# Performance work log

Measured on AMD Instinct MI355X. Metric: run time of the kernel, lower is better.

The kernel has to match this reference:

```python
import jax, jax.numpy as jnp
import numpy as np

B, S, E, H = 4, 1024, 1024, 16
HD = E // H


def setup_inputs() -> dict:
    key = jax.random.key(0)
    ks = jax.random.split(key, 5)
    x = jax.random.normal(ks[0], (B, S, E), dtype=jnp.float32)
    # causal mask: True = masked (filled with -inf), as in masked_fill_
    mask = jnp.triu(jnp.ones((S, S), dtype=bool), k=1)
    in_proj_weight = jax.random.normal(ks[1], (3 * E, E), dtype=jnp.float32) * (E ** -0.5)
    in_proj_bias = jax.random.normal(ks[2], (3 * E,), dtype=jnp.float32) * 0.02
    out_w = jax.random.normal(ks[3], (E, E), dtype=jnp.float32) * (E ** -0.5)
    out_b = jax.random.normal(ks[4], (E,), dtype=jnp.float32) * 0.02
    return {"x": x, "mask": mask, "in_proj_weight": in_proj_weight,
            "in_proj_bias": in_proj_bias, "out_w": out_w, "out_b": out_b}


def reference(x, mask, in_proj_weight, in_proj_bias, out_w, out_b):
    scaling = HD ** -0.5
    # fused QKV projection (self-attention path: qkv_same)
    qkv = jnp.einsum('bse,fe->bsf', x, in_proj_weight) + in_proj_bias  # [B,S,3E]
    q, k, v = jnp.split(qkv, 3, axis=-1)
    # split heads -> [B,H,S,HD]
    def heads(t):
        return t.reshape(B, S, H, HD).transpose(0, 2, 1, 3)
    q, k, v = heads(q), heads(k), heads(v)
    scores = jnp.einsum('bhsd,bhtd->bhst', q, k) * scaling  # [B,H,S,S]
    scores = jnp.where(mask[None, None, :, :], -jnp.inf, scores)
    att = jax.nn.softmax(scores, axis=-1)  # dropout p=0.0 (eval)
    out = jnp.einsum('bhst,bhtd->bhsd', att, v)  # [B,H,S,HD]
    out = out.transpose(0, 2, 1, 3).reshape(B, S, E)  # concat heads
    out = jnp.einsum('bse,fe->bsf', out, out_w) + out_b
    att_weights = att.reshape(B * H, S, S)
    return out, att_weights
```

## Files before the change

kernel.cpp:

```cpp
#include <hip/hip_runtime.h>
#include <hip/hip_bf16.h>
#include <stdint.h>

#define NH 16
#define SEQ 1024
#define EMB 1024
#define HDIM 64
#define BATCH 4
#define SPAD 1032

typedef float f32x4 __attribute__((ext_vector_type(4)));
typedef short bf16x8 __attribute__((ext_vector_type(8)));
typedef short bf16x4 __attribute__((ext_vector_type(4)));

static __device__ __forceinline__ short f2bf(float f) {
  union { float f; uint32_t u; } v; v.f = f;
  uint32_t r = (v.u + 0x7FFF + ((v.u >> 16) & 1)) >> 16;
  return (short)(uint16_t)r;
}
static __device__ __forceinline__ float bf2f(short h) {
  union { uint32_t u; float f; } v; v.u = ((uint32_t)(uint16_t)h) << 16;
  return v.f;
}

static __device__ __forceinline__ void gload_lds16(const void* g, void* l) {
  __builtin_amdgcn_global_load_lds(
      (const __attribute__((address_space(1))) void*)g,
      (__attribute__((address_space(3))) void*)l, 16, 0, 0);
}

static __device__ __forceinline__ void cvt8(const float* s, short* d) {
  const float4* sv = (const float4*)s;
  float4 a = sv[0], b = sv[1];
  bf16x8 o;
  o[0] = f2bf(a.x); o[1] = f2bf(a.y); o[2] = f2bf(a.z); o[3] = f2bf(a.w);
  o[4] = f2bf(b.x); o[5] = f2bf(b.y); o[6] = f2bf(b.z); o[7] = f2bf(b.w);
  *(bf16x8*)d = o;
}

__global__ void cvt3_kernel(const float* __restrict__ x, const float* __restrict__ w,
                            const float* __restrict__ o, short* __restrict__ xb,
                            short* __restrict__ wb, short* __restrict__ ob) {
  int i = (blockIdx.x * blockDim.x + threadIdx.x) * 8;
  if (i < 4194304) {
    cvt8(x + i, xb + i);
  } else if (i < 7340032) {
    cvt8(w + (i - 4194304), wb + (i - 4194304));
  } else {
    cvt8(o + (i - 7340032), ob + (i - 7340032));
  }
}

__global__ __launch_bounds__(256) void transpose_v(const short* __restrict__ v,
                                                   short* __restrict__ vt) {
  __shared__ short t[64][72];
  const int tid = threadIdx.x;
  const int bh = blockIdx.y;
  const int sb = blockIdx.x * 64;
  const int row = tid >> 2;
  const int c0 = (tid & 3) * 16;
  const short* src = v + ((size_t)(bh * SEQ + sb + row)) * HDIM + c0;
  *(bf16x8*)&t[row][c0] = *(const bf16x8*)src;
  *(bf16x8*)&t[row][c0 + 8] = *(const bf16x8*)(src + 8);
  __syncthreads();
  bf16x8 o0, o1;
#pragma unroll
  for (int i = 0; i < 8; ++i) o0[i] = t[c0 + i][row];
#pragma unroll
  for (int i = 0; i < 8; ++i) o1[i] = t[c0 + 8 + i][row];
  short* dst = vt + ((size_t)(bh * HDIM + row)) * SEQ + sb + c0;
  *(bf16x8*)dst = o0;
  *(bf16x8*)(dst + 8) = o1;
}

#define STAGE_QKV(bb, kk0)                                                     \
  {                                                                            \
    _Pragma("unroll") for (int c = 0; c < 2; ++c) {                            \
      int oo = o + c * 1024;                                                   \
      int row = oo >> 6;                                                       \
      int scol = (oo & 63) ^ ((row & 3) << 4);                                 \
      gload_lds16((const char*)A + ((size_t)(row0 + row) * K + (kk0)) * 2 + scol, \
                  (char*)As[bb] + (w * 2 + c) * 1024);                         \
      gload_lds16((const char*)Bm + ((size_t)(col0 + row) * K + (kk0)) * 2 + scol,\
                  (char*)Bs[bb] + (w * 2 + c) * 1024);                         \
    }                                                                          \
  }

#define COMPUTE_QKV(bb)                                                        \
  {                                                                            \
    bf16x8 af[4], bfr[4];                                                      \
    const int kbo = (l4 * 16) ^ ((l15 & 3) << 4);                              \
    _Pragma("unroll") for (int i = 0; i < 4; ++i) {                            \
      af[i] = *(const bf16x8*)((const char*)As[bb] + (wr * 64 + i * 16 + l15) * 64 + kbo); \
      bfr[i] = *(const bf16x8*)((const char*)Bs[bb] + (wc * 64 + i * 16 + l15) * 64 + kbo); \
    }                                                                          \
    _Pragma("unroll") for (int i = 0; i < 4; ++i)                              \
      _Pragma("unroll") for (int j = 0; j < 4; ++j)                            \
        acc[i][j] = __builtin_amdgcn_mfma_f32_16x16x32_bf16(af[i], bfr[j], acc[i][j], 0, 0, 0); \
  }

__global__ __launch_bounds__(256) void gemm_qkv(
    const short* __restrict__ A, const short* __restrict__ Bm,
    const float* __restrict__ bias, short* __restrict__ qkvws) {
  __shared__ short As[2][128 * 32];
  __shared__ short Bs[2][128 * 32];
  const int tid = threadIdx.x;
  const int w = tid >> 6, l = tid & 63;
  const int l15 = l & 15, l4 = l >> 4;
  const int wr = w >> 1, wc = w & 1;
  const int row0 = blockIdx.x * 128;
  const int col0 = blockIdx.y * 128;
  const int K = EMB;

  f32x4 acc[4][4] = {};

  const int o = (w * 2) * 1024 + l * 16;
  STAGE_QKV(0, 0);
  __syncthreads();

  int cur = 0;
  for (int k0 = 0; k0 < K; k0 += 32) {
    if (k0 + 32 < K) STAGE_QKV(cur ^ 1, k0 + 32);
    COMPUTE_QKV(cur);
    __syncthreads();
    cur ^= 1;
  }

#pragma unroll
  for (int j = 0; j < 4; ++j) {
    int f = col0 + wc * 64 + j * 16 + l15;
    float bv = bias[f];
    int part = f >> 10;
    int e = f & 1023;
    int hh = e >> 6, d = e & 63;
#pragma unroll
    for (int i = 0; i < 4; ++i) {
#pragma unroll
      for (int rr = 0; rr < 4; ++rr) {
        int m = row0 + wr * 64 + i * 16 + l4 * 4 + rr;
        int bb = m >> 10, ss = m & 1023;
        qkvws[(size_t)part * 4194304 +
              ((size_t)(bb * NH + hh) * SEQ + ss) * HDIM + d] =
            f2bf(acc[i][j][rr] + bv);
      }
    }
  }
}

#define STAGE_OUT(bb, kk0)                                                     \
  {                                                                            \
    _Pragma("unroll") for (int c = 0; c < 2; ++c) {                            \
      int oo = oA + c * 1024;                                                  \
      int row = oo >> 6;                                                       \
      int scol = (oo & 63) ^ ((row & 3) << 4);                                 \
      gload_lds16((const char*)A + ((size_t)(row0 + row) * K + (kk0)) * 2 + scol, \
                  (char*)As[bb] + (w * 2 + c) * 1024);                         \
    }                                                                          \
    {                                                                          \
      int oo = oB;                                                             \
      int row = oo >> 6;                                                       \
      int scol = (oo & 63) ^ ((row & 3) << 4);                                 \
      gload_lds16((const char*)Bm + ((size_t)(col0 + row) * K + (kk0)) * 2 + scol,\
                  (char*)Bs[bb] + w * 1024);                                   \
    }                                                                          \
  }

#define COMPUTE_OUT(bb)                                                        \
  {                                                                            \
    bf16x8 af[2], bfr[4];                                                      \
    const int kbo = (l4 * 16) ^ ((l15 & 3) << 4);                              \
    _Pragma("unroll") for (int i = 0; i < 2; ++i)                              \
      af[i] = *(const bf16x8*)((const char*)As[bb] + (w * 32 + i * 16 + l15) * 64 + kbo); \
    _Pragma("unroll") for (int j = 0; j < 4; ++j)                              \
      bfr[j] = *(const bf16x8*)((const char*)Bs[bb] + (j * 16 + l15) * 64 + kbo); \
    _Pragma("unroll") for (int i = 0; i < 2; ++i)                              \
      _Pragma("unroll") for (int j = 0; j < 4; ++j)                            \
        acc[i][j] = __builtin_amdgcn_mfma_f32_16x16x32_bf16(af[i], bfr[j], acc[i][j], 0, 0, 0); \
  }

__global__ __launch_bounds__(256) void gemm_out64(
    const short* __restrict__ A, const short* __restrict__ Bm,
    const float* __restrict__ bias, float* __restrict__ outp) {
  __shared__ short As[2][128 * 32];
  __shared__ short Bs[2][64 * 32];
  const int tid = threadIdx.x;
  const int w = tid >> 6, l = tid & 63;
  const int l15 = l & 15, l4 = l >> 4;
  const int row0 = blockIdx.x * 128;
  const int col0 = blockIdx.y * 64;
  const int K = EMB;

  f32x4 acc[2][4] = {};

  const int oA = (w * 2) * 1024 + l * 16;
  const int oB = w * 1024 + l * 16;
  STAGE_OUT(0, 0);
  __syncthreads();

  int cur = 0;
  for (int k0 = 0; k0 < K; k0 += 32) {
    if (k0 + 32 < K) STAGE_OUT(cur ^ 1, k0 + 32);
    COMPUTE_OUT(cur);
    __syncthreads();
    cur ^= 1;
  }

#pragma unroll
  for (int j = 0; j < 4; ++j) {
    int f = col0 + j * 16 + l15;
    float bv = bias[f];
#pragma unroll
    for (int i = 0; i < 2; ++i)
#pragma unroll
      for (int rr = 0; rr < 4; ++rr) {
        int m = row0 + w * 32 + i * 16 + l4 * 4 + rr;
        __builtin_nontemporal_store(acc[i][j][rr] + bv, &outp[(size_t)m * EMB + f]);
      }
  }
}

__global__ __launch_bounds__(256) void attn_kernel(
    const short* __restrict__ qws, const short* __restrict__ kws,
    const short* __restrict__ vtws, float* __restrict__ attg,
    short* __restrict__ aow) {
  __shared__ short strip[32 * SPAD];
  __shared__ float wsum[4][32];
  __shared__ float inv_sum[32];

  const int tid = threadIdx.x;
  const int w = tid >> 6, l = tid & 63;
  const int l15 = l & 15, l4 = l >> 4;
  const int blk = blockIdx.x;
  const int bh = blk >> 5;
  const int r = blk & 31;
  const int rowbase = r * 32;

  const short* qb = qws + ((size_t)bh * SEQ + rowbase) * HDIM;
  const short* kb = kws + (size_t)bh * SEQ * HDIM;
  const short* vb = vtws + (size_t)bh * HDIM * SEQ;
  float* ablk = attg + (size_t)bh * SEQ * SEQ + (size_t)rowbase * SEQ;

  bf16x8 qf[2][2];
#pragma unroll
  for (int rg = 0; rg < 2; ++rg)
#pragma unroll
    for (int ks = 0; ks < 2; ++ks)
      qf[rg][ks] = *(const bf16x8*)(qb + (rg * 16 + l15) * HDIM + ks * 32 + l4 * 8);

  const int ngroups = (rowbase + 32) >> 4;
  const int limit = ngroups * 16;
  float psum[2][4] = {};

  for (int g = w; g < ngroups; g += 4) {
    const short* kg = kb + (g * 16 + l15) * HDIM + l4 * 8;
    bf16x8 kf0 = *(const bf16x8*)(kg);
    bf16x8 kf1 = *(const bf16x8*)(kg + 32);
    f32x4 a0 = {}, a1 = {};
    a0 = __builtin_amdgcn_mfma_f32_16x16x32_bf16(qf[0][0], kf0, a0, 0, 0, 0);
    a0 = __builtin_amdgcn_mfma_f32_16x16x32_bf16(qf[0][1], kf1, a0, 0, 0, 0);
    a1 = __builtin_amdgcn_mfma_f32_16x16x32_bf16(qf[1][0], kf0, a1, 0, 0, 0);
    a1 = __builtin_amdgcn_mfma_f32_16x16x32_bf16(qf[1][1], kf1, a1, 0, 0, 0);
    int col = g * 16 + l15;
#pragma unroll
    for (int rg = 0; rg < 2; ++rg) {
#pragma unroll
      for (int rr = 0; rr < 4; ++rr) {
        int rloc = rg * 16 + l4 * 4 + rr;
        int row = rowbase + rloc;
        float sv = (rg ? a1[rr] : a0[rr]) * 0.125f;
        float ev = (col <= row) ? __expf(sv) : 0.0f;
        psum[rg][rr] += ev;
        strip[rloc * SPAD + col] = f2bf(ev);
      }
    }
  }

  {
    const int rloc = tid >> 3;
    const int cb = tid & 7;
    float* arow = ablk + (size_t)rloc * SEQ;
    const f32x4 z = (f32x4)0.0f;
    for (int c = limit + cb * 4; c < SEQ; c += 32)
      __builtin_nontemporal_store(z, (f32x4*)(arow + c));
  }

#pragma unroll
  for (int rg = 0; rg < 2; ++rg)
#pragma unroll
    for (int rr = 0; rr < 4; ++rr) {
      float v = psum[rg][rr];
      v += __shfl_xor(v, 1);
      v += __shfl_xor(v, 2);
      v += __shfl_xor(v, 4);
      v += __shfl_xor(v, 8);
      psum[rg][rr] = v;
    }
  if (l15 == 0) {
#pragma unroll
    for (int rg = 0; rg < 2; ++rg)
#pragma unroll
      for (int rr = 0; rr < 4; ++rr)
        wsum[w][rg * 16 + l4 * 4 + rr] = psum[rg][rr];
  }
  __syncthreads();
  if (tid < 32) {
    float s = wsum[0][tid] + wsum[1][tid] + wsum[2][tid] + wsum[3][tid];
    inv_sum[tid] = 1.0f / s;
  }
  __syncthreads();

  {
    const int nch = ngroups >> 1;
    const int d0 = w * 16;
    const int wrloc = tid >> 3;
    const int wcb = tid & 7;
    const float wisr = inv_sum[wrloc];
    float* warow = ablk + (size_t)wrloc * SEQ;
    f32x4 oacc[2] = {};
    const short* vrow = vb + (d0 + l15) * SEQ + l4 * 8;
    for (int c = 0; c < nch; ++c) {
      bf16x8 vf = *(const bf16x8*)(vrow + c * 32);
      bf16x8 p0 = *(const bf16x8*)&strip[(0 + l15) * SPAD + c * 32 + l4 * 8];
      bf16x8 p1 = *(const bf16x8*)&strip[(16 + l15) * SPAD + c * 32 + l4 * 8];
      oacc[0] = __builtin_amdgcn_mfma_f32_16x16x32_bf16(p0, vf, oacc[0], 0, 0, 0);
      oacc[1] = __builtin_amdgcn_mfma_f32_16x16x32_bf16(p1, vf, oacc[1], 0, 0, 0);
      {
        int col = c * 32 + wcb * 4;
        bf16x4 pw = *(const bf16x4*)&strip[wrloc * SPAD + col];
        f32x4 ov;
        ov[0] = bf2f(pw[0]) * wisr; ov[1] = bf2f(pw[1]) * wisr;
        ov[2] = bf2f(pw[2]) * wisr; ov[3] = bf2f(pw[3]) * wisr;
        __builtin_nontemporal_store(ov, (f32x4*)(warow + col));
      }
    }
    const int b = bh >> 4, h = bh & 15;
#pragma unroll
    for (int rg = 0; rg < 2; ++rg) {
#pragma unroll
      for (int rr = 0; rr < 4; ++rr) {
        int rloc = rg * 16 + l4 * 4 + rr;
        int s = rowbase + rloc;
        float v = oacc[rg][rr] * inv_sum[rloc];
        aow[((size_t)(b * SEQ + s)) * EMB + h * HDIM + d0 + l15] = f2bf(v);
      }
    }
  }
}

extern "C" void kernel_launch(void* const* d_in, const int* in_sizes, int n_in,
                              void* d_out, int out_size, void* d_ws, size_t ws_size,
                              hipStream_t stream) {
  (void)in_sizes; (void)n_in; (void)out_size; (void)ws_size;
  const float* x = (const float*)d_in[0];
  const float* ipw = (const float*)d_in[2];
  const float* ipb = (const float*)d_in[3];
  const float* ow = (const float*)d_in[4];
  const float* ob = (const float*)d_in[5];
  float* outp = (float*)d_out;
  float* attg = (float*)d_out + (size_t)BATCH * SEQ * EMB;

  char* ws = (char*)d_ws;
  short* xbf = (short*)(ws);
  short* wbf = (short*)(ws + 8388608);
  short* owbf = (short*)(ws + 14680064);
  short* qkvws = (short*)(ws + 16777216);
  short* aow = (short*)(ws + 41943040);
  short* vtws = (short*)(ws);

  short* qws = qkvws;
  short* kws = qkvws + 4194304;
  short* vws = qkvws + 8388608;

  cvt3_kernel<<<4096, 256, 0, stream>>>(x, ipw, ow, xbf, wbf, owbf);

  dim3 g1(32, 24);
  gemm_qkv<<<g1, 256, 0, stream>>>(xbf, wbf, ipb, qkvws);

  transpose_v<<<dim3(16, 64), 256, 0, stream>>>(vws, vtws);

  attn_kernel<<<2048, 256, 0, stream>>>(qws, kws, vtws, attg, aow);

  gemm_out64<<<dim3(32, 16), 256, 0, stream>>>(aow, owbf, ob, outp);
}
```

Before: 150.9 us.

## Fuse V transpose into QKV GEMM epilogue and hoist zero-fill stores

The QKV GEMM epilogue now writes the V part directly in transposed [B,H,D,S] layout using 4-element vector stores, which removes the separate transpose_v kernel launch and its extra read and write of V. Separately, in the attention kernel, the nontemporal zero-fill of the masked upper region of the attention matrix is moved ahead of the QK loop so those stores can overlap with compute. The transposed V stores are strided across the sequence dimension, so coalescing in the epilogue may be worse than before.

Result: no change. 152.5 us (+1.0%).

```diff
diff --git a/kernel.cpp b/kernel.cpp
--- a/kernel.cpp
+++ b/kernel.cpp
@@ -49,28 +49,6 @@
   } else {
     cvt8(o + (i - 7340032), ob + (i - 7340032));
   }
-}
-
-__global__ __launch_bounds__(256) void transpose_v(const short* __restrict__ v,
-                                                   short* __restrict__ vt) {
-  __shared__ short t[64][72];
-  const int tid = threadIdx.x;
-  const int bh = blockIdx.y;
-  const int sb = blockIdx.x * 64;
-  const int row = tid >> 2;
-  const int c0 = (tid & 3) * 16;
-  const short* src = v + ((size_t)(bh * SEQ + sb + row)) * HDIM + c0;
-  *(bf16x8*)&t[row][c0] = *(const bf16x8*)src;
-  *(bf16x8*)&t[row][c0 + 8] = *(const bf16x8*)(src + 8);
-  __syncthreads();
-  bf16x8 o0, o1;
-#pragma unroll
-  for (int i = 0; i < 8; ++i) o0[i] = t[c0 + i][row];
-#pragma unroll
-  for (int i = 0; i < 8; ++i) o1[i] = t[c0 + 8 + i][row];
-  short* dst = vt + ((size_t)(bh * HDIM + row)) * SEQ + sb + c0;
-  *(bf16x8*)dst = o0;
-  *(bf16x8*)(dst + 8) = o1;
 }
 
 #define STAGE_QKV(bb, kk0)                                                     \
@@ -126,6 +104,7 @@
     cur ^= 1;
   }
 
+  short* vt = qkvws + 8388608;
 #pragma unroll
   for (int j = 0; j < 4; ++j) {
     int f = col0 + wc * 64 + j * 16 + l15;
@@ -133,15 +112,27 @@
     int part = f >> 10;
     int e = f & 1023;
     int hh = e >> 6, d = e & 63;
-#pragma unroll
-    for (int i = 0; i < 4; ++i) {
-#pragma unroll
-      for (int rr = 0; rr < 4; ++rr) {
-        int m = row0 + wr * 64 + i * 16 + l4 * 4 + rr;
-        int bb = m >> 10, ss = m & 1023;
-        qkvws[(size_t)part * 4194304 +
-              ((size_t)(bb * NH + hh) * SEQ + ss) * HDIM + d] =
-            f2bf(acc[i][j][rr] + bv);
+    if (part < 2) {
+#pragma unroll
+      for (int i = 0; i < 4; ++i) {
+#pragma unroll
+        for (int rr = 0; rr < 4; ++rr) {
+          int m = row0 + wr * 64 + i * 16 + l4 * 4 + rr;
+          int bb = m >> 10, ss = m & 1023;
+          qkvws[(size_t)part * 4194304 +
+                ((size_t)(bb * NH + hh) * SEQ + ss) * HDIM + d] =
+              f2bf(acc[i][j][rr] + bv);
+        }
+      }
+    } else {
+#pragma unroll
+      for (int i = 0; i < 4; ++i) {
+        int m0 = row0 + wr * 64 + i * 16 + l4 * 4;
+        int bb = m0 >> 10, ss0 = m0 & 1023;
+        bf16x4 pv;
+#pragma unroll
+        for (int rr = 0; rr < 4; ++rr) pv[rr] = f2bf(acc[i][j][rr] + bv);
+        *(bf16x4*)&vt[((size_t)(bb * NH + hh) * HDIM + d) * SEQ + ss0] = pv;
       }
     }
   }
@@ -240,6 +231,18 @@
   const short* vb = vtws + (size_t)bh * HDIM * SEQ;
   float* ablk = attg + (size_t)bh * SEQ * SEQ + (size_t)rowbase * SEQ;
 
+  const int ngroups = (rowbase + 32) >> 4;
+  const int limit = ngroups * 16;
+
+  {
+    const int rloc = tid >> 3;
+    const int cb = tid & 7;
+    float* arow = ablk + (size_t)rloc * SEQ;
+    const f32x4 z = (f32x4)0.0f;
+    for (int c = limit + cb * 4; c < SEQ; c += 32)
+      __builtin_nontemporal_store(z, (f32x4*)(arow + c));
+  }
+
   bf16x8 qf[2][2];
 #pragma unroll
   for (int rg = 0; rg < 2; ++rg)
@@ -247,8 +250,6 @@
     for (int ks = 0; ks < 2; ++ks)
       qf[rg][ks] = *(const bf16x8*)(qb + (rg * 16 + l15) * HDIM + ks * 32 + l4 * 8);
 
-  const int ngroups = (rowbase + 32) >> 4;
-  const int limit = ngroups * 16;
   float psum[2][4] = {};
 
   for (int g = w; g < ngroups; g += 4) {
@@ -273,15 +274,6 @@
         strip[rloc * SPAD + col] = f2bf(ev);
       }
     }
-  }
-
-  {
-    const int rloc = tid >> 3;
-    const int cb = tid & 7;
-    float* arow = ablk + (size_t)rloc * SEQ;
-    const f32x4 z = (f32x4)0.0f;
-    for (int c = limit + cb * 4; c < SEQ; c += 32)
-      __builtin_nontemporal_store(z, (f32x4*)(arow + c));
   }
 
 #pragma unroll
@@ -365,19 +357,16 @@
   short* owbf = (short*)(ws + 14680064);
   short* qkvws = (short*)(ws + 16777216);
   short* aow = (short*)(ws + 41943040);
-  short* vtws = (short*)(ws);
 
   short* qws = qkvws;
   short* kws = qkvws + 4194304;
-  short* vws = qkvws + 8388608;
+  short* vtws = qkvws + 8388608;
 
   cvt3_kernel<<<4096, 256, 0, stream>>>(x, ipw, ow, xbf, wbf, owbf);
 
   dim3 g1(32, 24);
   gemm_qkv<<<g1, 256, 0, stream>>>(xbf, wbf, ipb, qkvws);
 
-  transpose_v<<<dim3(16, 64), 256, 0, stream>>>(vws, vtws);
-
   attn_kernel<<<2048, 256, 0, stream>>>(qws, kws, vtws, attg, aow);
 
   gemm_out64<<<dim3(32, 16), 256, 0, stream>>>(aow, owbf, ob, outp);
```
